# Kernel tuning notes

Hardware: AMD Instinct MI355X
Metric: run time of the kernel (lower is better)

## Reference

```python
import jax, jax.numpy as jnp
import numpy as np

ANCHORS = np.array([[116, 90], [156, 198], [373, 326],
                    [30, 61], [62, 45], [59, 119],
                    [10, 13], [16, 30], [33, 23]], dtype=np.float32)
IMG = 416.0
NUM_CLASSES = 80
IGNORE_THR = 0.5
SUB_BY_S = {13: 0, 26: 3, 52: 6}  # subtract_index per feature size


def setup_inputs() -> dict:
    key = jax.random.key(0)
    k1, k2, k3, k4 = jax.random.split(key, 4)
    B, N, S = 32, 32, 52
    output = jax.random.normal(k1, (B, 255, S, S), dtype=jnp.float32)
    xy = jax.random.uniform(k2, (B, N, 2), minval=10.0, maxval=406.0)
    wh = jax.random.uniform(k3, (B, N, 2), minval=10.0, maxval=120.0)
    cls = jax.random.randint(k4, (B, N, 1), 0, NUM_CLASSES).astype(jnp.float32)
    targets = jnp.concatenate([xy, wh, cls], axis=-1)  # [B, N, 5] pixel units
    return {"output": output, "targets": targets}


def _bce(p, t):
    eps = 1e-7
    p = jnp.clip(p, eps, 1.0 - eps)
    return -t * jnp.log(p) - (1.0 - t) * jnp.log(1.0 - p)


def _yolo_loss(output, targets):
    B, _, S, _ = output.shape
    C = NUM_CLASSES
    stride = IMG / S
    scaled = jnp.asarray(ANCHORS) / stride          # [9,2] anchors in feature units
    sub = SUB_BY_S[S]

    pred = output.reshape(B, 3, 5 + C, S, S).transpose(0, 1, 3, 4, 2)  # [B,3,S,S,85]
    x = jax.nn.sigmoid(pred[..., 0])
    y = jax.nn.sigmoid(pred[..., 1])
    w = pred[..., 2]
    h = pred[..., 3]
    conf = jax.nn.sigmoid(pred[..., 4])
    pred_cls = jax.nn.sigmoid(pred[..., 5:])

    # ---- get_target (vectorized anchor matching + scatter into grid) ----
    gx = targets[..., 0] / stride                    # [B,N]
    gy = targets[..., 1] / stride
    gw = targets[..., 2] / stride
    gh = targets[..., 3] / stride
    gi = jnp.floor(gx).astype(jnp.int32)
    gj = jnp.floor(gy).astype(jnp.int32)

    aw, ah = scaled[:, 0], scaled[:, 1]              # [9]
    # IoU of (0,0,gw,gh) vs (0,0,aw,ah): centered boxes -> overlap = min(w)*min(h)
    inter = jnp.minimum(gw[..., None], aw) * jnp.minimum(gh[..., None], ah)
    union = gw[..., None] * gh[..., None] + aw * ah - inter
    best = jnp.argmax(inter / union, axis=-1)        # [B,N] best of 9 anchors
    valid = (best >= sub) & (best < sub + 3)
    k = best - sub

    size = B * 3 * S * S
    bidx = jnp.arange(B, dtype=jnp.int32)[:, None]
    flat = (((bidx * 3 + k) * S + gj) * S + gi)      # [i, best_n-sub, gj, gi]
    flat = jnp.where(valid, flat, size)              # sentinel -> dropped
    fr = flat.ravel()

    def scat(vals):
        return jnp.zeros(size, jnp.float32).at[fr].set(
            vals.ravel(), mode='drop').reshape(B, 3, S, S)

    mask = scat(jnp.ones_like(gx))
    noobj = jnp.ones(size, jnp.float32).at[fr].set(0.0, mode='drop').reshape(B, 3, S, S)
    tx = scat(gx - gi.astype(jnp.float32))
    ty = scat(gy - gj.astype(jnp.float32))
    tw = scat(jnp.log(gw / scaled[best, 0]))
    th = scat(jnp.log(gh / scaled[best, 1]))
    bls_x = scat(targets[..., 2] / IMG)
    bls_y = scat(targets[..., 3] / IMG)

    cls_id = targets[..., 4].astype(jnp.int32)
    flat_c = jnp.where(valid, flat * C + cls_id, size * C)
    tcls = jnp.zeros(size * C, jnp.float32).at[flat_c.ravel()].set(
        1.0, mode='drop').reshape(B, 3, S, S, C)

    # ---- get_ignore (pred boxes vs gt boxes, IoU threshold mask) ----
    grid = jnp.arange(S, dtype=jnp.float32)
    la = scaled[sub:sub + 3]                         # [3,2] layer anchors
    px = x + grid[None, None, None, :]
    py = y + grid[None, None, :, None]
    pw = jnp.exp(w) * la[:, 0][None, :, None, None]
    ph = jnp.exp(h) * la[:, 1][None, :, None, None]
    pb = jax.lax.stop_gradient(
        jnp.stack([px, py, pw, ph], axis=-1).reshape(B, -1, 4))  # [B,M,4]

    ax1, ax2 = gx - gw / 2, gx + gw / 2              # [B,N]
    ay1, ay2 = gy - gh / 2, gy + gh / 2
    bx1 = pb[..., 0] - pb[..., 2] / 2                # [B,M]
    bx2 = pb[..., 0] + pb[..., 2] / 2
    by1 = pb[..., 1] - pb[..., 3] / 2
    by2 = pb[..., 1] + pb[..., 3] / 2
    iw = jnp.clip(jnp.minimum(ax2[:, :, None], bx2[:, None, :]) -
                  jnp.maximum(ax1[:, :, None], bx1[:, None, :]), 0.0)
    ih = jnp.clip(jnp.minimum(ay2[:, :, None], by2[:, None, :]) -
                  jnp.maximum(ay1[:, :, None], by1[:, None, :]), 0.0)
    inter2 = iw * ih                                 # [B,N,M]
    area_a = (gw * gh)[:, :, None]
    area_b = (pb[..., 2] * pb[..., 3])[:, None, :]
    iou = inter2 / (area_a + area_b - inter2)
    iou_max = jnp.max(iou, axis=1).reshape(B, 3, S, S)
    noobj = jnp.where(iou_max > IGNORE_THR, 0.0, noobj)

    # ---- losses ----
    box_loss_scale = 2.0 - bls_x * bls_y
    loss_x = jnp.sum(_bce(x, tx) / B * box_loss_scale * mask)
    loss_y = jnp.sum(_bce(y, ty) / B * box_loss_scale * mask)
    loss_w = jnp.sum((w - tw) ** 2 / B * 0.5 * box_loss_scale * mask)
    loss_h = jnp.sum((h - th) ** 2 / B * 0.5 * box_loss_scale * mask)
    bce_conf = _bce(conf, mask)
    loss_conf = jnp.sum(bce_conf * mask / B) + jnp.sum(bce_conf * noobj / B)
    loss_cls = jnp.sum(_bce(pred_cls, tcls) * mask[..., None] / B)

    loss = loss_x + loss_y + loss_w + loss_h + loss_conf + loss_cls
    num_pos = jnp.maximum(jnp.sum(mask), 1.0)
    return loss, num_pos


def reference(output, targets):
    return _yolo_loss(output, targets)
```

## Files before the change

kernel.cpp:

```cpp
#include <hip/hip_runtime.h>
#include <hip/hip_bf16.h>

#define B_    32
#define N_    32
#define S_    52
#define C_    80
#define PLANE (S_*S_)
#define CPB   (3*PLANE)
#define TOT   (B_*CPB)
#define NBLK  (TOT/256)

__device__ __constant__ float d_aw[9] = {14.5f, 19.5f, 46.625f, 3.75f, 7.75f, 7.375f, 1.25f, 2.0f,  4.125f};
__device__ __constant__ float d_ah[9] = {11.25f,24.75f,40.75f,  7.625f,5.625f,14.875f,1.625f,3.75f, 2.875f};

__global__ void kzero(float* res) {
    if (threadIdx.x < 2) res[threadIdx.x] = 0.0f;
}
__global__ void kfix(float* res) {
    res[1] = fmaxf(res[1], 1.0f);
}

__device__ __forceinline__ float sigm(float z)  { return 1.0f / (1.0f + __expf(-z)); }
__device__ __forceinline__ float clampp(float p){ return fminf(fmaxf(p, 1e-7f), 1.0f - 1e-7f); }

__launch_bounds__(256)
__global__ void kmain(const float* __restrict__ pred,
                      const float* __restrict__ tgts,
                      float2* __restrict__ part,
                      float* __restrict__ res,
                      int use_part) {
    __shared__ float4 s_box[64];
    __shared__ float2 s_am[64];
    __shared__ float4 s_reg[64];
    __shared__ float  s_bls[64];
    __shared__ float  s_red[8];

    const int g   = blockIdx.x*256 + (int)threadIdx.x;
    const int b   = g / CPB;
    const int r   = g - b*CPB;
    const int a   = r / PLANE;
    const int lin = r - a*PLANE;
    const int i   = lin / S_;
    const int j   = lin - i*S_;

    const int off5 = (b*255 + a*85)*PLANE + lin;
    const float z0 = pred[off5];
    const float z1 = pred[off5 + 1*PLANE];
    const float z2 = pred[off5 + 2*PLANE];
    const float z3 = pred[off5 + 3*PLANE];
    const float z4 = pred[off5 + 4*PLANE];

    const int bFirst = (blockIdx.x*256) / CPB;
    const int bLast  = (blockIdx.x*256 + 255) / CPB;
    const int nb     = bLast - bFirst + 1;
    if ((int)threadIdx.x < nb * 32) {
        const int n  = threadIdx.x & 31;
        const int bb = bFirst + ((int)threadIdx.x >> 5);
        const float* tp = tgts + (size_t)(bb*N_ + n)*5;
        const float t0 = tp[0], t1 = tp[1], t2 = tp[2], t3 = tp[3], t4 = tp[4];
        const float gx = t0*0.125f, gy = t1*0.125f, gw = t2*0.125f, gh = t3*0.125f;
        int best = 0; float bestr = -1.0f;
        #pragma unroll
        for (int cc = 0; cc < 9; cc++) {
            const float inter = fminf(gw, d_aw[cc]) * fminf(gh, d_ah[cc]);
            const float uni   = gw*gh + d_aw[cc]*d_ah[cc] - inter;
            const float rr    = inter / uni;
            if (rr > bestr) { bestr = rr; best = cc; }
        }
        const int valid = (best >= 6 && best < 9) ? 1 : 0;
        const int gi = (int)floorf(gx);
        const int gj = (int)floorf(gy);
        const int key = valid ? (((best - 6) << 12) | (gj << 6) | gi) : 16383;
        const int meta = key | (((int)t4) << 14);
        s_box[threadIdx.x] = make_float4(gx - gw*0.5f, gy - gh*0.5f, gx + gw*0.5f, gy + gh*0.5f);
        s_am[threadIdx.x]  = make_float2(gw * gh, __int_as_float(meta));
        s_reg[threadIdx.x] = make_float4(gx - (float)gi, gy - (float)gj,
                                         __logf(gw / d_aw[best]), __logf(gh / d_ah[best]));
        s_bls[threadIdx.x] = 2.0f - (t2*(1.0f/416.0f))*(t3*(1.0f/416.0f));
    }
    __syncthreads();

    const float la_w = (a == 0) ? 1.25f  : ((a == 1) ? 2.0f  : 4.125f);
    const float la_h = (a == 0) ? 1.625f : ((a == 1) ? 3.75f : 2.875f);
    const float sx = sigm(z0);
    const float sy = sigm(z1);
    const float px = sx + (float)j;
    const float py = sy + (float)i;
    const float pw = __expf(z2) * la_w;
    const float ph = __expf(z3) * la_h;
    const float bx1 = px - pw*0.5f, bx2 = px + pw*0.5f;
    const float by1 = py - ph*0.5f, by2 = py + ph*0.5f;
    const float areab = pw * ph;

    bool ignore = false;
    int  lastm  = -1;
    unsigned long long cm_lo = 0ull;
    unsigned int       cm_hi = 0u;
    const int sbase = (b - bFirst) * 32;
    const int mykey = (a << 12) | (i << 6) | j;
    #pragma unroll 8
    for (int n = 0; n < N_; n++) {
        const float4 tb = s_box[sbase+n];
        const float2 am = s_am[sbase+n];
        const int  meta = __float_as_int(am.y);
        const float iw = fmaxf(fminf(tb.z, bx2) - fmaxf(tb.x, bx1), 0.0f);
        const float ih = fmaxf(fminf(tb.w, by2) - fmaxf(tb.y, by1), 0.0f);
        const float inter = iw * ih;
        ignore = ignore || (3.0f*inter > am.x + areab);
        if ((meta & 16383) == mykey) {
            lastm = n;
            const int mcls = meta >> 14;
            if (mcls < 64) cm_lo |= 1ull << mcls;
            else           cm_hi |= 1u << (mcls - 64);
        }
    }

    const float invB = 1.0f / (float)B_;
    float loss = 0.0f, npos = 0.0f;

    const float conf = clampp(sigm(z4));
    if (lastm < 0) {
        if (!ignore) loss = -__logf(1.0f - conf) * invB;
    } else {
        npos = 1.0f;
        const float4 rg  = s_reg[sbase + lastm];
        const float  bls = s_bls[sbase + lastm];
        const float x = clampp(sx);
        const float y = clampp(sy);
        const float bx = -rg.x*__logf(x) - (1.0f - rg.x)*__logf(1.0f - x);
        const float by = -rg.y*__logf(y) - (1.0f - rg.y)*__logf(1.0f - y);
        const float dw = z2 - rg.z;
        const float dh = z3 - rg.w;
        loss = (-__logf(conf) + (bx + by + 0.5f*dw*dw + 0.5f*dh*dh) * bls) * invB;
    }

    {
        unsigned long long pm = __ballot(lastm >= 0);
        const int lane = (int)(threadIdx.x & 63);
        const int myoff = off5 + 5*PLANE;
        float clsacc = 0.0f;
        while (pm) {
            const int src = __ffsll((unsigned long long)pm) - 1;
            pm &= pm - 1;
            const int soff          = __shfl(myoff, src, 64);
            const unsigned int slo0 = (unsigned int)__shfl((int)(cm_lo & 0xffffffffull), src, 64);
            const unsigned int slo1 = (unsigned int)__shfl((int)(cm_lo >> 32), src, 64);
            const unsigned int shi  = (unsigned int)__shfl((int)cm_hi, src, 64);
            const float za = pred[soff + lane*PLANE];
            const float pa = clampp(sigm(za));
            const bool  ta = (lane < 32) ? ((slo0 >> lane) & 1u) : ((slo1 >> (lane - 32)) & 1u);
            clsacc += ta ? -__logf(pa) : -__logf(1.0f - pa);
            if (lane < 16) {
                const float zb = pred[soff + (64 + lane)*PLANE];
                const float pb = clampp(sigm(zb));
                const bool  tb = (shi >> lane) & 1u;
                clsacc += tb ? -__logf(pb) : -__logf(1.0f - pb);
            }
        }
        loss += clsacc * invB;
    }

    #pragma unroll
    for (int off = 32; off > 0; off >>= 1) {
        loss += __shfl_down(loss, off, 64);
        npos += __shfl_down(npos, off, 64);
    }
    if ((threadIdx.x & 63) == 0) {
        s_red[(threadIdx.x >> 6)*2 + 0] = loss;
        s_red[(threadIdx.x >> 6)*2 + 1] = npos;
    }
    __syncthreads();
    if (threadIdx.x == 0) {
        float L = 0.0f, P = 0.0f;
        #pragma unroll
        for (int w = 0; w < 4; w++) { L += s_red[2*w]; P += s_red[2*w+1]; }
        if (use_part) part[blockIdx.x] = make_float2(L, P);
        else { atomicAdd(res + 0, L); atomicAdd(res + 1, P); }
    }
}

__launch_bounds__(256)
__global__ void kfinal(const float2* __restrict__ part, float* __restrict__ res) {
    __shared__ float s_red[8];
    float L = 0.0f, P = 0.0f;
    for (int k = threadIdx.x; k < NBLK; k += 256) {
        const float2 v = part[k];
        L += v.x; P += v.y;
    }
    #pragma unroll
    for (int off = 32; off > 0; off >>= 1) {
        L += __shfl_down(L, off, 64);
        P += __shfl_down(P, off, 64);
    }
    if ((threadIdx.x & 63) == 0) {
        s_red[(threadIdx.x >> 6)*2 + 0] = L;
        s_red[(threadIdx.x >> 6)*2 + 1] = P;
    }
    __syncthreads();
    if (threadIdx.x == 0) {
        float tl = 0.0f, tp = 0.0f;
        #pragma unroll
        for (int w = 0; w < 4; w++) { tl += s_red[2*w]; tp += s_red[2*w+1]; }
        res[0] = tl;
        res[1] = fmaxf(tp, 1.0f);
    }
}

extern "C" void kernel_launch(void* const* d_in, const int* in_sizes, int n_in,
                              void* d_out, int out_size, void* d_ws, size_t ws_size,
                              hipStream_t stream) {
    const float* pred = (const float*)d_in[0];
    const float* tgts = (const float*)d_in[1];
    float* res = (float*)d_out;

    if (ws_size >= (size_t)NBLK * sizeof(float2)) {
        float2* part = (float2*)d_ws;
        kmain<<<NBLK, 256, 0, stream>>>(pred, tgts, part, res, 1);
        kfinal<<<1, 256, 0, stream>>>(part, res);
    } else {
        kzero<<<1, 64, 0, stream>>>(res);
        kmain<<<NBLK, 256, 0, stream>>>(pred, tgts, nullptr, res, 0);
        kfix<<<1, 1, 0, stream>>>(res);
    }
}
```

Measured before the change: 120.9 us.

## Process two cells per thread with one image per block

Each block now covers a single image with 16 blocks per image, and each thread handles two grid cells. The per-block target preprocessing runs once for 32 targets instead of up to 64, and the shared-memory target reads in the IoU loop are reused for both cells. Ten loads are issued up front per thread for more memory-level parallelism. The cost is higher register pressure, a tail of invalid slots in the last block of each image, and half as many blocks.

```diff
diff --git a/kernel.cpp b/kernel.cpp
--- a/kernel.cpp
+++ b/kernel.cpp
@@ -1,5 +1,4 @@
 #include <hip/hip_runtime.h>
-#include <hip/hip_bf16.h>
 
 #define B_    32
 #define N_    32
@@ -7,8 +6,8 @@
 #define C_    80
 #define PLANE (S_*S_)
 #define CPB   (3*PLANE)
-#define TOT   (B_*CPB)
-#define NBLK  (TOT/256)
+#define BPB   16
+#define NBLK  (B_*BPB)
 
 __device__ __constant__ float d_aw[9] = {14.5f, 19.5f, 46.625f, 3.75f, 7.75f, 7.375f, 1.25f, 2.0f,  4.125f};
 __device__ __constant__ float d_ah[9] = {11.25f,24.75f,40.75f,  7.625f,5.625f,14.875f,1.625f,3.75f, 2.875f};
@@ -29,33 +28,37 @@
                       float2* __restrict__ part,
                       float* __restrict__ res,
                       int use_part) {
-    __shared__ float4 s_box[64];
-    __shared__ float2 s_am[64];
-    __shared__ float4 s_reg[64];
-    __shared__ float  s_bls[64];
+    __shared__ float4 s_box[N_];
+    __shared__ float2 s_am[N_];
+    __shared__ float4 s_reg[N_];
+    __shared__ float  s_bls[N_];
     __shared__ float  s_red[8];
 
-    const int g   = blockIdx.x*256 + (int)threadIdx.x;
-    const int b   = g / CPB;
-    const int r   = g - b*CPB;
-    const int a   = r / PLANE;
-    const int lin = r - a*PLANE;
-    const int i   = lin / S_;
-    const int j   = lin - i*S_;
-
-    const int off5 = (b*255 + a*85)*PLANE + lin;
-    const float z0 = pred[off5];
-    const float z1 = pred[off5 + 1*PLANE];
-    const float z2 = pred[off5 + 2*PLANE];
-    const float z3 = pred[off5 + 3*PLANE];
-    const float z4 = pred[off5 + 4*PLANE];
-
-    const int bFirst = (blockIdx.x*256) / CPB;
-    const int bLast  = (blockIdx.x*256 + 255) / CPB;
-    const int nb     = bLast - bFirst + 1;
-    if ((int)threadIdx.x < nb * 32) {
-        const int n  = threadIdx.x & 31;
-        const int bb = bFirst + ((int)threadIdx.x >> 5);
+    const int bb = (int)blockIdx.x >> 4;
+    const int r0 = (((int)blockIdx.x & 15) << 9) + (int)threadIdx.x;
+    const int r1 = r0 + 256;
+    const bool v1 = (r1 < CPB);
+
+    const int a0 = r0 / PLANE, lin0 = r0 - a0*PLANE;
+    const int i0 = lin0 / S_,  j0 = lin0 - i0*S_;
+    const int a1t = r1 / PLANE, lin1 = r1 - a1t*PLANE;
+    const int i1 = lin1 / S_,  j1 = lin1 - i1*S_;
+
+    const int off0 = (bb*255 + a0*85)*PLANE + lin0;
+    const int off1 = v1 ? (bb*255 + a1t*85)*PLANE + lin1 : off0;
+    const float z00 = pred[off0];
+    const float z01 = pred[off0 + 1*PLANE];
+    const float z02 = pred[off0 + 2*PLANE];
+    const float z03 = pred[off0 + 3*PLANE];
+    const float z04 = pred[off0 + 4*PLANE];
+    const float z10 = pred[off1];
+    const float z11 = pred[off1 + 1*PLANE];
+    const float z12 = pred[off1 + 2*PLANE];
+    const float z13 = pred[off1 + 3*PLANE];
+    const float z14 = pred[off1 + 4*PLANE];
+
+    if ((int)threadIdx.x < N_) {
+        const int n  = (int)threadIdx.x;
         const float* tp = tgts + (size_t)(bb*N_ + n)*5;
         const float t0 = tp[0], t1 = tp[1], t2 = tp[2], t3 = tp[3], t4 = tp[4];
         const float gx = t0*0.125f, gy = t1*0.125f, gw = t2*0.125f, gh = t3*0.125f;
@@ -70,91 +73,132 @@
         const int valid = (best >= 6 && best < 9) ? 1 : 0;
         const int gi = (int)floorf(gx);
         const int gj = (int)floorf(gy);
-        const int key = valid ? (((best - 6) << 12) | (gj << 6) | gi) : 16383;
+        const int key  = valid ? (((best - 6) << 12) | (gj << 6) | gi) : 16383;
         const int meta = key | (((int)t4) << 14);
-        s_box[threadIdx.x] = make_float4(gx - gw*0.5f, gy - gh*0.5f, gx + gw*0.5f, gy + gh*0.5f);
-        s_am[threadIdx.x]  = make_float2(gw * gh, __int_as_float(meta));
-        s_reg[threadIdx.x] = make_float4(gx - (float)gi, gy - (float)gj,
-                                         __logf(gw / d_aw[best]), __logf(gh / d_ah[best]));
-        s_bls[threadIdx.x] = 2.0f - (t2*(1.0f/416.0f))*(t3*(1.0f/416.0f));
+        s_box[n] = make_float4(gx - gw*0.5f, gy - gh*0.5f, gx + gw*0.5f, gy + gh*0.5f);
+        s_am[n]  = make_float2(gw * gh, __int_as_float(meta));
+        s_reg[n] = make_float4(gx - (float)gi, gy - (float)gj,
+                               __logf(gw / d_aw[best]), __logf(gh / d_ah[best]));
+        s_bls[n] = 2.0f - (t2*(1.0f/416.0f))*(t3*(1.0f/416.0f));
     }
     __syncthreads();
 
-    const float la_w = (a == 0) ? 1.25f  : ((a == 1) ? 2.0f  : 4.125f);
-    const float la_h = (a == 0) ? 1.625f : ((a == 1) ? 3.75f : 2.875f);
-    const float sx = sigm(z0);
-    const float sy = sigm(z1);
-    const float px = sx + (float)j;
-    const float py = sy + (float)i;
-    const float pw = __expf(z2) * la_w;
-    const float ph = __expf(z3) * la_h;
-    const float bx1 = px - pw*0.5f, bx2 = px + pw*0.5f;
-    const float by1 = py - ph*0.5f, by2 = py + ph*0.5f;
-    const float areab = pw * ph;
-
-    bool ignore = false;
-    int  lastm  = -1;
-    unsigned long long cm_lo = 0ull;
-    unsigned int       cm_hi = 0u;
-    const int sbase = (b - bFirst) * 32;
-    const int mykey = (a << 12) | (i << 6) | j;
-    #pragma unroll 8
+    const float la_w0 = (a0 == 0) ? 1.25f  : ((a0 == 1) ? 2.0f  : 4.125f);
+    const float la_h0 = (a0 == 0) ? 1.625f : ((a0 == 1) ? 3.75f : 2.875f);
+    const float la_w1 = (a1t == 0) ? 1.25f  : ((a1t == 1) ? 2.0f  : 4.125f);
+    const float la_h1 = (a1t == 0) ? 1.625f : ((a1t == 1) ? 3.75f : 2.875f);
+
+    const float sx0 = sigm(z00), sy0 = sigm(z01);
+    const float px0 = sx0 + (float)j0, py0 = sy0 + (float)i0;
+    const float pw0 = __expf(z02) * la_w0, ph0 = __expf(z03) * la_h0;
+    const float bx10 = px0 - pw0*0.5f, bx20 = px0 + pw0*0.5f;
+    const float by10 = py0 - ph0*0.5f, by20 = py0 + ph0*0.5f;
+    const float ab0  = pw0 * ph0;
+
+    const float sx1 = sigm(z10), sy1 = sigm(z11);
+    const float px1 = sx1 + (float)j1, py1 = sy1 + (float)i1;
+    const float pw1 = __expf(z12) * la_w1, ph1 = __expf(z13) * la_h1;
+    const float bx11 = px1 - pw1*0.5f, bx21 = px1 + pw1*0.5f;
+    const float by11 = py1 - ph1*0.5f, by21 = py1 + ph1*0.5f;
+    const float ab1  = pw1 * ph1;
+
+    bool ig0 = false, ig1 = false;
+    int  lm0 = -1,    lm1 = -1;
+    unsigned long long c0lo = 0ull, c1lo = 0ull;
+    unsigned int       c0hi = 0u,   c1hi = 0u;
+    const int key0 = (a0  << 12) | (i0 << 6) | j0;
+    const int key1 = (a1t << 12) | (i1 << 6) | j1;
+    #pragma unroll 4
     for (int n = 0; n < N_; n++) {
-        const float4 tb = s_box[sbase+n];
-        const float2 am = s_am[sbase+n];
+        const float4 tb = s_box[n];
+        const float2 am = s_am[n];
         const int  meta = __float_as_int(am.y);
-        const float iw = fmaxf(fminf(tb.z, bx2) - fmaxf(tb.x, bx1), 0.0f);
-        const float ih = fmaxf(fminf(tb.w, by2) - fmaxf(tb.y, by1), 0.0f);
-        const float inter = iw * ih;
-        ignore = ignore || (3.0f*inter > am.x + areab);
-        if ((meta & 16383) == mykey) {
-            lastm = n;
-            const int mcls = meta >> 14;
-            if (mcls < 64) cm_lo |= 1ull << mcls;
-            else           cm_hi |= 1u << (mcls - 64);
-        }
-    }
+        const int  tkey = meta & 16383;
+        const int  mcls = meta >> 14;
+        const unsigned long long blo = (mcls < 64) ? (1ull << mcls) : 0ull;
+        const unsigned int       bhi = (mcls >= 64) ? (1u << (mcls - 64)) : 0u;
+        {
+            const float iw = fmaxf(fminf(tb.z, bx20) - fmaxf(tb.x, bx10), 0.0f);
+            const float ih = fmaxf(fminf(tb.w, by20) - fmaxf(tb.y, by10), 0.0f);
+            const float inter = iw * ih;
+            ig0 = ig0 || (3.0f*inter > am.x + ab0);
+            if (tkey == key0) { lm0 = n; c0lo |= blo; c0hi |= bhi; }
+        }
+        {
+            const float iw = fmaxf(fminf(tb.z, bx21) - fmaxf(tb.x, bx11), 0.0f);
+            const float ih = fmaxf(fminf(tb.w, by21) - fmaxf(tb.y, by11), 0.0f);
+            const float inter = iw * ih;
+            ig1 = ig1 || (3.0f*inter > am.x + ab1);
+            if (tkey == key1) { lm1 = n; c1lo |= blo; c1hi |= bhi; }
+        }
+    }
+    if (!v1) lm1 = -1;
 
     const float invB = 1.0f / (float)B_;
     float loss = 0.0f, npos = 0.0f;
 
-    const float conf = clampp(sigm(z4));
-    if (lastm < 0) {
-        if (!ignore) loss = -__logf(1.0f - conf) * invB;
-    } else {
-        npos = 1.0f;
-        const float4 rg  = s_reg[sbase + lastm];
-        const float  bls = s_bls[sbase + lastm];
-        const float x = clampp(sx);
-        const float y = clampp(sy);
-        const float bx = -rg.x*__logf(x) - (1.0f - rg.x)*__logf(1.0f - x);
-        const float by = -rg.y*__logf(y) - (1.0f - rg.y)*__logf(1.0f - y);
-        const float dw = z2 - rg.z;
-        const float dh = z3 - rg.w;
-        loss = (-__logf(conf) + (bx + by + 0.5f*dw*dw + 0.5f*dh*dh) * bls) * invB;
-    }
-
     {
-        unsigned long long pm = __ballot(lastm >= 0);
+        const float conf = clampp(sigm(z04));
+        if (lm0 < 0) {
+            if (!ig0) loss = -__logf(1.0f - conf) * invB;
+        } else {
+            npos = 1.0f;
+            const float4 rg  = s_reg[lm0];
+            const float  bls = s_bls[lm0];
+            const float x = clampp(sx0);
+            const float y = clampp(sy0);
+            const float bx = -rg.x*__logf(x) - (1.0f - rg.x)*__logf(1.0f - x);
+            const float by = -rg.y*__logf(y) - (1.0f - rg.y)*__logf(1.0f - y);
+            const float dw = z02 - rg.z;
+            const float dh = z03 - rg.w;
+            loss = (-__logf(conf) + (bx + by + 0.5f*dw*dw + 0.5f*dh*dh) * bls) * invB;
+        }
+    }
+    if (v1) {
+        const float conf = clampp(sigm(z14));
+        if (lm1 < 0) {
+            if (!ig1) loss += -__logf(1.0f - conf) * invB;
+        } else {
+            npos += 1.0f;
+            const float4 rg  = s_reg[lm1];
+            const float  bls = s_bls[lm1];
+            const float x = clampp(sx1);
+            const float y = clampp(sy1);
+            const float bx = -rg.x*__logf(x) - (1.0f - rg.x)*__logf(1.0f - x);
+            const float by = -rg.y*__logf(y) - (1.0f - rg.y)*__logf(1.0f - y);
+            const float dw = z12 - rg.z;
+            const float dh = z13 - rg.w;
+            loss += (-__logf(conf) + (bx + by + 0.5f*dw*dw + 0.5f*dh*dh) * bls) * invB;
+        }
+    }
+
+    {
         const int lane = (int)(threadIdx.x & 63);
-        const int myoff = off5 + 5*PLANE;
         float clsacc = 0.0f;
-        while (pm) {
-            const int src = __ffsll((unsigned long long)pm) - 1;
-            pm &= pm - 1;
-            const int soff          = __shfl(myoff, src, 64);
-            const unsigned int slo0 = (unsigned int)__shfl((int)(cm_lo & 0xffffffffull), src, 64);
-            const unsigned int slo1 = (unsigned int)__shfl((int)(cm_lo >> 32), src, 64);
-            const unsigned int shi  = (unsigned int)__shfl((int)cm_hi, src, 64);
-            const float za = pred[soff + lane*PLANE];
-            const float pa = clampp(sigm(za));
-            const bool  ta = (lane < 32) ? ((slo0 >> lane) & 1u) : ((slo1 >> (lane - 32)) & 1u);
-            clsacc += ta ? -__logf(pa) : -__logf(1.0f - pa);
-            if (lane < 16) {
-                const float zb = pred[soff + (64 + lane)*PLANE];
-                const float pb = clampp(sigm(zb));
-                const bool  tb = (shi >> lane) & 1u;
-                clsacc += tb ? -__logf(pb) : -__logf(1.0f - pb);
+        #pragma unroll
+        for (int slot = 0; slot < 2; slot++) {
+            const int lm = (slot == 0) ? lm0 : lm1;
+            const int myoff = ((slot == 0) ? off0 : off1) + 5*PLANE;
+            const unsigned long long mlo = (slot == 0) ? c0lo : c1lo;
+            const unsigned int       mhi = (slot == 0) ? c0hi : c1hi;
+            unsigned long long pm = __ballot(lm >= 0);
+            while (pm) {
+                const int src = __ffsll((unsigned long long)pm) - 1;
+                pm &= pm - 1;
+                const int soff          = __shfl(myoff, src, 64);
+                const unsigned int slo0 = (unsigned int)__shfl((int)(mlo & 0xffffffffull), src, 64);
+                const unsigned int slo1 = (unsigned int)__shfl((int)(mlo >> 32), src, 64);
+                const unsigned int shi  = (unsigned int)__shfl((int)mhi, src, 64);
+                const float za = pred[soff + lane*PLANE];
+                const float pa = clampp(sigm(za));
+                const bool  ta = (lane < 32) ? ((slo0 >> lane) & 1u) : ((slo1 >> (lane - 32)) & 1u);
+                clsacc += ta ? -__logf(pa) : -__logf(1.0f - pa);
+                if (lane < 16) {
+                    const float zb = pred[soff + (64 + lane)*PLANE];
+                    const float pb = clampp(sigm(zb));
+                    const bool  tb2 = (shi >> lane) & 1u;
+                    clsacc += tb2 ? -__logf(pb) : -__logf(1.0f - pb);
+                }
             }
         }
         loss += clsacc * invB;
```

After: 120.9 us. About the same (+0.1%).
